# Kernel tuning notes

Hardware: AMD Instinct MI355X
Metric: run time of the kernel (lower is better)

## Reference

```python
import jax, jax.numpy as jnp
import numpy as np

PADDING_VALUE = 0.0  # padding_value init arg


def setup_inputs() -> dict:
    key = jax.random.key(0)
    k1, k2 = jax.random.split(key)
    B, T, D = 16, 4096, 256
    x = jax.random.normal(k1, (B, T, D), dtype=jnp.float32)
    mask = jax.random.bernoulli(k2, 0.5, (B, T))  # bool
    return {"x": x, "mask": mask}


def reference(x, mask):
    # batch_first=True: x is [B, T, ...feat], mask is [B, T].
    B, T = mask.shape
    lens = mask.sum(axis=1)  # [B] number of selected elements per row
    # Stable argsort on (~mask) brings indices of True entries to the front,
    # preserving their original order -> index of the j-th True element.
    order = jnp.argsort(jnp.logical_not(mask), axis=1, stable=True)  # [B, T]
    # Gather x rows into compacted order.
    idx = order.reshape(order.shape + (1,) * (x.ndim - 2))  # [B, T, 1...]
    gathered = jnp.take_along_axis(x, idx, axis=1)  # [B, T, ...feat]
    # Right-pad positions j >= lens[b] with padding_value.
    valid = jnp.arange(T)[None, :] < lens[:, None]  # [B, T]
    valid = valid.reshape(valid.shape + (1,) * (x.ndim - 2))
    x_ = jnp.where(valid, gathered, jnp.asarray(PADDING_VALUE, x.dtype))
    return x_, lens
```

## Files before the change

### kernel.cpp

```cpp
#include <hip/hip_runtime.h>


typedef float f32x4 __attribute__((ext_vector_type(4)));

#define BLK 256
#define NW (BLK / 64)
#define ROWS 64
#define PF 12

template <int NITER>
__global__ __launch_bounds__(BLK, 4) void pad_masked_pipe(
    const float* __restrict__ x,
    const int* __restrict__ mask,
    float* __restrict__ out,
    float* __restrict__ lens_f,
    int T, int D4) {

    const int b = blockIdx.x;
    const int c = blockIdx.y;
    const int tid = threadIdx.x;
    const int lane = tid & 63;
    const int wave = tid >> 6;
    const int j0 = c * ROWS;

    const int* mrow = mask + (size_t)b * T;

    const int msel = (mrow[j0 + lane] != 0);

    int4 mv[NITER];
    #pragma unroll
    for (int k = 0; k < NITER; ++k)
        mv[k] = *reinterpret_cast<const int4*>(mrow + (size_t)(tid + k * BLK) * 4);

    const unsigned long long sel = __ballot(msel);
    const f32x4* xrow = reinterpret_cast<const f32x4*>(x) +
                        ((size_t)b * T + j0) * (size_t)D4;

    unsigned long long t = sel;
    #pragma unroll
    for (int k = 0; k < NW - 1; ++k)
        if (k < wave) t &= t - 1;

    f32x4 v[PF];
    int cnt = 0;
    #pragma unroll
    for (int k = 0; k < PF; ++k) {
        if (t) {
            const int r = (int)__builtin_ctzll(t);
            v[k] = xrow[(size_t)r * 64 + lane];
            cnt = k + 1;
            #pragma unroll
            for (int p = 0; p < NW; ++p) t &= t - 1;
        }
    }

    int pre = 0, all = 0;
    #pragma unroll
    for (int k = 0; k < NITER; ++k) {
        const int4 m4 = mv[k];
        const int s4 = (m4.x != 0) + (m4.y != 0) + (m4.z != 0) + (m4.w != 0);
        all += s4;
        if ((tid + k * BLK) * 4 < j0) pre += s4;
    }
    unsigned long long packed = (unsigned long long)(unsigned)pre |
                                ((unsigned long long)(unsigned)all << 32);
    #pragma unroll
    for (int off = 32; off; off >>= 1) packed += __shfl_xor(packed, off);

    __shared__ unsigned long long wred[NW];
    if (lane == 0) wred[wave] = packed;
    __syncthreads();
    unsigned long long tot = 0;
    #pragma unroll
    for (int w = 0; w < NW; ++w) tot += wred[w];
    const int P = (int)(tot & 0xffffffffull);
    const int L = (int)(tot >> 32);

    if (c == 0 && tid == 0) lens_f[b] = (float)L;

    f32x4* obase = reinterpret_cast<f32x4*>(out) + (size_t)b * T * (size_t)D4;
    #pragma unroll
    for (int k = 0; k < PF; ++k)
        if (k < cnt)
            obase[(size_t)(P + wave + k * NW) * 64 + lane] = v[k];
    int i = wave + PF * NW;
    while (t) {
        const int r = (int)__builtin_ctzll(t);
        #pragma unroll
        for (int p = 0; p < NW; ++p) t &= t - 1;
        obase[(size_t)(P + i) * 64 + lane] = xrow[(size_t)r * 64 + lane];
        i += NW;
    }

    const f32x4 z = {0.f, 0.f, 0.f, 0.f};
    const int zstart = (L > j0) ? L : j0;
    for (int j = zstart + wave; j < j0 + ROWS; j += NW)
        obase[(size_t)j * 64 + lane] = z;
}

__global__ __launch_bounds__(BLK) void pad_masked_fused(
    const float* __restrict__ x,
    const int* __restrict__ mask,
    float* __restrict__ out,
    float* __restrict__ lens_f,
    int T, int D4) {

    const int b = blockIdx.x;
    const int c = blockIdx.y;
    const int tid = threadIdx.x;
    const int lane = tid & 63;
    const int wave = tid >> 6;
    const int j0 = c * ROWS;

    const int* mrow = mask + (size_t)b * T;

    int pre = 0, all = 0;
    for (int e = tid * 4; e < T; e += BLK * 4) {
        const int4 mv = *reinterpret_cast<const int4*>(mrow + e);
        const int s4 = (mv.x != 0) + (mv.y != 0) + (mv.z != 0) + (mv.w != 0);
        all += s4;
        if (e < j0) pre += s4;
    }
    unsigned long long packed = (unsigned long long)(unsigned)pre |
                                ((unsigned long long)(unsigned)all << 32);
    #pragma unroll
    for (int off = 32; off; off >>= 1) packed += __shfl_xor(packed, off);

    __shared__ unsigned long long wred[NW];
    __shared__ int selRows[ROWS];
    __shared__ int nsel;
    if (lane == 0) wred[wave] = packed;
    __syncthreads();
    unsigned long long tot = 0;
    #pragma unroll
    for (int w = 0; w < NW; ++w) tot += wred[w];
    const int P = (int)(tot & 0xffffffffull);
    const int L = (int)(tot >> 32);

    if (wave == 0) {
        const int m = (mrow[j0 + lane] != 0);
        int incl = m;
        #pragma unroll
        for (int off = 1; off < 64; off <<= 1) {
            const int v = __shfl_up(incl, off);
            if (lane >= off) incl += v;
        }
        if (m) selRows[incl - 1] = lane;
        if (lane == 63) nsel = incl;
    }
    __syncthreads();
    const int n = nsel;

    if (c == 0 && tid == 0) lens_f[b] = (float)L;

    const f32x4* xrow = reinterpret_cast<const f32x4*>(x) +
                        ((size_t)b * T + j0) * (size_t)D4;
    f32x4* obase = reinterpret_cast<f32x4*>(out) + (size_t)b * T * (size_t)D4;
    const f32x4 z = {0.f, 0.f, 0.f, 0.f};

    for (int i = wave; i < n; i += 2 * NW) {
        const int i2 = i + NW;
        const bool h2 = (i2 < n);
        const int r0 = selRows[i];
        const int r1 = h2 ? selRows[i2] : 0;
        for (int tt = lane; tt < D4; tt += 64) {
            const f32x4 v0 = xrow[(size_t)r0 * D4 + tt];
            f32x4 v1 = z;
            if (h2) v1 = xrow[(size_t)r1 * D4 + tt];
            obase[(size_t)(P + i) * D4 + tt] = v0;
            if (h2) obase[(size_t)(P + i2) * D4 + tt] = v1;
        }
    }

    const int zstart = (L > j0) ? L : j0;
    for (int j = zstart + wave; j < j0 + ROWS; j += NW)
        for (int tt = lane; tt < D4; tt += 64)
            obase[(size_t)j * D4 + tt] = z;
}

extern "C" void kernel_launch(void* const* d_in, const int* in_sizes, int n_in,
                              void* d_out, int out_size, void* d_ws, size_t ws_size,
                              hipStream_t stream) {
    const float* x = (const float*)d_in[0];
    const int* mask = (const int*)d_in[1];

    const int Nx = in_sizes[0];
    const int BT = in_sizes[1];
    const int B = out_size - Nx;
    const int T = BT / B;
    const int D = Nx / BT;
    const int D4 = D / 4;

    float* out = (float*)d_out;
    float* lens_f = out + (size_t)Nx;

    dim3 grid(B, T / ROWS);

    const int niter = T / (BLK * 4);
    const bool fast = (D4 == 64) && (T % (BLK * 4) == 0) && (T % ROWS == 0);
    if (fast && niter == 4)
        pad_masked_pipe<4><<<grid, BLK, 0, stream>>>(x, mask, out, lens_f, T, D4);
    else if (fast && niter == 2)
        pad_masked_pipe<2><<<grid, BLK, 0, stream>>>(x, mask, out, lens_f, T, D4);
    else if (fast && niter == 1)
        pad_masked_pipe<1><<<grid, BLK, 0, stream>>>(x, mask, out, lens_f, T, D4);
    else if (fast && niter == 8)
        pad_masked_pipe<8><<<grid, BLK, 0, stream>>>(x, mask, out, lens_f, T, D4);
    else
        pad_masked_fused<<<grid, BLK, 0, stream>>>(x, mask, out, lens_f, T, D4);
}
```

Measured before the change: 19.66 us.

## Balance zero-fill across chunks and make row prefetch branch-free

Each chunk block now writes its own share of padding zeros, at positions counted back from the end of the row using its prefix count P and selected count n. Before, zero writes piled up in the trailing chunks. The full-row count reduction is dropped, and lens is written by the last chunk as P+n. Row indices are computed first and all PF prefetch loads are issued without branches. Lanes with no row left reload row 0, which adds some redundant loads in exchange for more memory parallelism.

```diff
diff --git a/kernel.cpp b/kernel.cpp
--- a/kernel.cpp
+++ b/kernel.cpp
@@ -14,7 +14,7 @@
     const int* __restrict__ mask,
     float* __restrict__ out,
     float* __restrict__ lens_f,
-    int T, int D4) {
+    int T, int CPB) {
 
     const int b = blockIdx.x;
     const int c = blockIdx.y;
@@ -33,52 +33,48 @@
         mv[k] = *reinterpret_cast<const int4*>(mrow + (size_t)(tid + k * BLK) * 4);
 
     const unsigned long long sel = __ballot(msel);
+    const int n = (int)__popcll(sel);
+
     const f32x4* xrow = reinterpret_cast<const f32x4*>(x) +
-                        ((size_t)b * T + j0) * (size_t)D4;
-
+                        ((size_t)b * T + j0) * (size_t)64;
     unsigned long long t = sel;
     #pragma unroll
     for (int k = 0; k < NW - 1; ++k)
         if (k < wave) t &= t - 1;
 
+    int rk[PF];
+    {
+        unsigned long long u = t;
+        #pragma unroll
+        for (int k = 0; k < PF; ++k) {
+            rk[k] = u ? (int)__builtin_ctzll(u) : 0;
+            #pragma unroll
+            for (int p = 0; p < NW; ++p) u &= u - 1;
+        }
+        t = u;
+    }
     f32x4 v[PF];
-    int cnt = 0;
-    #pragma unroll
-    for (int k = 0; k < PF; ++k) {
-        if (t) {
-            const int r = (int)__builtin_ctzll(t);
-            v[k] = xrow[(size_t)r * 64 + lane];
-            cnt = k + 1;
-            #pragma unroll
-            for (int p = 0; p < NW; ++p) t &= t - 1;
-        }
-    }
-
-    int pre = 0, all = 0;
+    #pragma unroll
+    for (int k = 0; k < PF; ++k)
+        v[k] = xrow[(size_t)rk[k] * 64 + lane];
+
+    int pre = 0;
     #pragma unroll
     for (int k = 0; k < NITER; ++k) {
         const int4 m4 = mv[k];
-        const int s4 = (m4.x != 0) + (m4.y != 0) + (m4.z != 0) + (m4.w != 0);
-        all += s4;
-        if ((tid + k * BLK) * 4 < j0) pre += s4;
-    }
-    unsigned long long packed = (unsigned long long)(unsigned)pre |
-                                ((unsigned long long)(unsigned)all << 32);
-    #pragma unroll
-    for (int off = 32; off; off >>= 1) packed += __shfl_xor(packed, off);
-
-    __shared__ unsigned long long wred[NW];
-    if (lane == 0) wred[wave] = packed;
+        const int e = (tid + k * BLK) * 4;
+        if (e < j0) pre += (m4.x != 0) + (m4.y != 0) + (m4.z != 0) + (m4.w != 0);
+    }
+    #pragma unroll
+    for (int off = 32; off; off >>= 1) pre += __shfl_xor(pre, off);
+
+    __shared__ int wred[NW];
+    if (lane == 0) wred[wave] = pre;
     __syncthreads();
-    unsigned long long tot = 0;
-    #pragma unroll
-    for (int w = 0; w < NW; ++w) tot += wred[w];
-    const int P = (int)(tot & 0xffffffffull);
-    const int L = (int)(tot >> 32);
-
-    if (c == 0 && tid == 0) lens_f[b] = (float)L;
-
-    f32x4* obase = reinterpret_cast<f32x4*>(out) + (size_t)b * T * (size_t)D4;
+    const int P = wred[0] + wred[1] + wred[2] + wred[3];
+
+    f32x4* obase = reinterpret_cast<f32x4*>(out) + (size_t)b * T * (size_t)64;
+    const int cnt = (n > wave) ? ((n - wave - 1) / NW + 1) : 0;
     #pragma unroll
     for (int k = 0; k < PF; ++k)
         if (k < cnt)
@@ -93,9 +89,11 @@
     }
 
     const f32x4 z = {0.f, 0.f, 0.f, 0.f};
-    const int zstart = (L > j0) ? L : j0;
-    for (int j = zstart + wave; j < j0 + ROWS; j += NW)
+    const int pend = T - c * ROWS + P;
+    for (int j = pend - (ROWS - n) + wave; j < pend; j += NW)
         obase[(size_t)j * 64 + lane] = z;
+
+    if (c == CPB - 1 && tid == 0) lens_f[b] = (float)(P + n);
 }
 
 __global__ __launch_bounds__(BLK) void pad_masked_fused(
@@ -142,8 +140,8 @@
         int incl = m;
         #pragma unroll
         for (int off = 1; off < 64; off <<= 1) {
-            const int v = __shfl_up(incl, off);
-            if (lane >= off) incl += v;
+            const int vv = __shfl_up(incl, off);
+            if (lane >= off) incl += vv;
         }
         if (m) selRows[incl - 1] = lane;
         if (lane == 63) nsel = incl;
@@ -158,18 +156,10 @@
     f32x4* obase = reinterpret_cast<f32x4*>(out) + (size_t)b * T * (size_t)D4;
     const f32x4 z = {0.f, 0.f, 0.f, 0.f};
 
-    for (int i = wave; i < n; i += 2 * NW) {
-        const int i2 = i + NW;
-        const bool h2 = (i2 < n);
+    for (int i = wave; i < n; i += NW) {
         const int r0 = selRows[i];
-        const int r1 = h2 ? selRows[i2] : 0;
-        for (int tt = lane; tt < D4; tt += 64) {
-            const f32x4 v0 = xrow[(size_t)r0 * D4 + tt];
-            f32x4 v1 = z;
-            if (h2) v1 = xrow[(size_t)r1 * D4 + tt];
-            obase[(size_t)(P + i) * D4 + tt] = v0;
-            if (h2) obase[(size_t)(P + i2) * D4 + tt] = v1;
-        }
+        for (int tt = lane; tt < D4; tt += 64)
+            obase[(size_t)(P + i) * D4 + tt] = xrow[(size_t)r0 * D4 + tt];
     }
 
     const int zstart = (L > j0) ? L : j0;
@@ -190,22 +180,23 @@
     const int T = BT / B;
     const int D = Nx / BT;
     const int D4 = D / 4;
+    const int CPB = T / ROWS;
 
     float* out = (float*)d_out;
     float* lens_f = out + (size_t)Nx;
 
-    dim3 grid(B, T / ROWS);
+    dim3 grid(B, CPB);
 
     const int niter = T / (BLK * 4);
     const bool fast = (D4 == 64) && (T % (BLK * 4) == 0) && (T % ROWS == 0);
     if (fast && niter == 4)
-        pad_masked_pipe<4><<<grid, BLK, 0, stream>>>(x, mask, out, lens_f, T, D4);
+        pad_masked_pipe<4><<<grid, BLK, 0, stream>>>(x, mask, out, lens_f, T, CPB);
     else if (fast && niter == 2)
-        pad_masked_pipe<2><<<grid, BLK, 0, stream>>>(x, mask, out, lens_f, T, D4);
+        pad_masked_pipe<2><<<grid, BLK, 0, stream>>>(x, mask, out, lens_f, T, CPB);
     else if (fast && niter == 1)
-        pad_masked_pipe<1><<<grid, BLK, 0, stream>>>(x, mask, out, lens_f, T, D4);
+        pad_masked_pipe<1><<<grid, BLK, 0, stream>>>(x, mask, out, lens_f, T, CPB);
     else if (fast && niter == 8)
-        pad_masked_pipe<8><<<grid, BLK, 0, stream>>>(x, mask, out, lens_f, T, D4);
+        pad_masked_pipe<8><<<grid, BLK, 0, stream>>>(x, mask, out, lens_f, T, CPB);
     else
         pad_masked_fused<<<grid, BLK, 0, stream>>>(x, mask, out, lens_f, T, D4);
 }
```

New measurement: 19.43 us. Within noise of the previous version (-1.2%).
